# Optimization experiments

Measured on AMD Instinct MI355X. Metric: run time of the kernel, lower is better.

The kernel has to match this reference:

```python
import jax, jax.numpy as jnp
import numpy as np

N = 50000      # nodes
E = 1600000    # edges
F = 128        # num_feature
H = 256        # num_hidden
L = 3          # num_message_passing_steps
EPS = 1e-5     # LayerNorm eps (torch default)


def setup_inputs() -> dict:
    key = jax.random.key(0)
    ks = jax.random.split(key, 8)
    node = jax.random.normal(ks[0], (N, F), dtype=jnp.float32)
    edges = jax.random.randint(ks[1], (2, E), 0, N, dtype=jnp.int64)
    edges_attr = jax.random.uniform(ks[2], (E,), dtype=jnp.float32)
    sF = np.float32(1.0 / np.sqrt(F))
    sH = np.float32(1.0 / np.sqrt(H))
    W1 = jax.random.normal(ks[3], (F, H), dtype=jnp.float32) * sF
    b1 = jnp.zeros((H,), jnp.float32)
    W_convs = jax.random.normal(ks[4], (L, H, H), dtype=jnp.float32) * sH
    b_convs = jnp.zeros((L, H), jnp.float32)
    ln_g = jnp.ones((L, H), jnp.float32)
    ln_b = jnp.zeros((L, H), jnp.float32)
    fc_W = jax.random.normal(ks[5], (H, 2), dtype=jnp.float32) * sH
    fc_b = jnp.zeros((2,), jnp.float32)
    return dict(node=node, edges=edges, edges_attr=edges_attr, W1=W1, b1=b1,
                W_convs=W_convs, b_convs=b_convs, ln_g=ln_g, ln_b=ln_b,
                fc_W=fc_W, fc_b=fc_b)


def gcn_conv(x, src_a, dst_a, w_a, W, b):
    # PyG GCNConv: x' = D^-1/2 (A + I) D^-1/2 (x W) + b, edge weights w.
    # src_a/dst_a/w_a already include self-loops (weight 1).
    n = x.shape[0]
    xw = x @ W                                      # [N, H]
    deg = jax.ops.segment_sum(w_a, dst_a, num_segments=n)
    deg_safe = jnp.where(deg > 0, deg, 1.0)
    dinv = jnp.where(deg > 0, jax.lax.rsqrt(deg_safe), 0.0)
    norm = dinv[src_a] * w_a * dinv[dst_a]          # [E+N]
    msg = xw[src_a] * norm[:, None]                 # gather + scale
    out = jax.ops.segment_sum(msg, dst_a, num_segments=n)  # scatter-add
    return out + b


def layer_norm(x, g, b):
    mu = jnp.mean(x, axis=-1, keepdims=True)
    var = jnp.mean((x - mu) ** 2, axis=-1, keepdims=True)
    return (x - mu) * jax.lax.rsqrt(var + EPS) * g + b


def reference(node, edges, edges_attr, W1, b1, W_convs, b_convs, ln_g, ln_b, fc_W, fc_b):
    n = node.shape[0]
    loop = jnp.arange(n, dtype=edges.dtype)
    src_a = jnp.concatenate([edges[0], loop])
    dst_a = jnp.concatenate([edges[1], loop])
    w_a = jnp.concatenate([edges_attr, jnp.ones((n,), edges_attr.dtype)])

    x = gcn_conv(node, src_a, dst_a, w_a, W1, b1)
    for i in range(L):
        x_res = x
        x = gcn_conv(x, src_a, dst_a, w_a, W_convs[i], b_convs[i])
        x = layer_norm(x, ln_g[i], ln_b[i])
        x = jax.nn.relu(x + x_res)
    x = x @ fc_W + fc_b                              # [N, 2]
    return jnp.mean(x, axis=0, keepdims=True)        # global_mean_pool, batch=None -> [1, 2]
```

## Files before the change

### kernel.cpp

```cpp
#include <hip/hip_runtime.h>

#define EPS 1e-5f
#define FIXSCALE 8388608.0f

typedef __attribute__((ext_vector_type(8))) short short8;
typedef __attribute__((ext_vector_type(4))) short short4v;
typedef __attribute__((ext_vector_type(4))) float float4v;
typedef __attribute__((ext_vector_type(8))) unsigned short ushort8;
typedef __attribute__((ext_vector_type(4))) unsigned int uint4v;

#if __has_builtin(__builtin_nontemporal_load)
#define NT_LOAD(p) __builtin_nontemporal_load(p)
#else
#define NT_LOAD(p) (*(p))
#endif

__device__ __forceinline__ unsigned short f2b(float f) {
    union { float f; unsigned u; } v; v.f = f;
    unsigned r = v.u + 0x7FFF + ((v.u >> 16) & 1);
    return (unsigned short)(r >> 16);
}
__device__ __forceinline__ float b2f(unsigned short u) {
    union { unsigned u; float f; } v; v.u = ((unsigned)u) << 16;
    return v.f;
}


__global__ __launch_bounds__(256) void rank_kernel(const int* __restrict__ dst,
                                                   const float* __restrict__ w,
                                                   unsigned long long* __restrict__ combo,
                                                   int* __restrict__ rank, int E) {
    int e = blockIdx.x * 256 + threadIdx.x;
    if (e < E) {
        int d = dst[e];
        unsigned long long pack = (1ULL << 32) | (unsigned long long)(unsigned)(w[e] * FIXSCALE);
        unsigned long long old = atomicAdd(&combo[(size_t)d * 8], pack);
        rank[e] = (int)(old >> 32);
    }
}

__global__ __launch_bounds__(1024) void scan_dinv_kernel(const unsigned long long* __restrict__ combo,
                                                         int* __restrict__ row_ptr,
                                                         float* __restrict__ dinv, int n) {
    int tid = threadIdx.x, lane = tid & 63, w = tid >> 6;
    __shared__ int wsum[16];
    __shared__ int s_carry;
    if (tid == 0) s_carry = 0;
    __syncthreads();
    for (int base = 0; base < n; base += 1024) {
        int i = base + tid;
        int v = 0;
        if (i < n) {
            unsigned long long cb = combo[(size_t)i * 8];
            int cnt = (int)(cb >> 32);
            v = (cnt + 4) & ~3;
            float degv = (float)(unsigned)(cb & 0xffffffffULL) * (1.0f / FIXSCALE);
            dinv[i] = rsqrtf(degv + 1.0f);
        }
        int x = v;
        for (int off = 1; off < 64; off <<= 1) {
            int t = __shfl_up(x, off);
            if (lane >= off) x += t;
        }
        if (lane == 63) wsum[w] = x;
        __syncthreads();
        if (w == 0 && lane < 16) {
            int s = wsum[lane];
            for (int off = 1; off < 16; off <<= 1) {
                int t = __shfl_up(s, off, 16);
                if (lane >= off) s += t;
            }
            wsum[lane] = s;
        }
        __syncthreads();
        int carry = s_carry;
        int woff = (w > 0) ? wsum[w - 1] : 0;
        if (i < n) row_ptr[i + 1] = carry + woff + x;
        __syncthreads();
        if (tid == 0) s_carry = carry + wsum[15];
        __syncthreads();
    }
    if (tid == 0) row_ptr[0] = 0;
}

__global__ __launch_bounds__(256) void selfpad_kernel(const unsigned long long* __restrict__ combo,
                                                      const int* __restrict__ row_ptr,
                                                      const float* __restrict__ dinv,
                                                      unsigned int* __restrict__ edge, int n) {
    int d = blockIdx.x * 256 + threadIdx.x;
    if (d < n) {
        int cnt = (int)(combo[(size_t)d * 8] >> 32);
        int j0 = row_ptr[d], j1 = row_ptr[d + 1];
        float di = dinv[d];
        edge[j0] = ((unsigned)f2b(di * di) << 16) | (unsigned)d;
        for (int j = j0 + 1 + cnt; j < j1; ++j) edge[j] = (unsigned)d;
    }
}

__global__ __launch_bounds__(256) void scatter2_kernel(
    const int* __restrict__ src, const int* __restrict__ dst,
    const float* __restrict__ w, const int* __restrict__ rank,
    const int* __restrict__ row_ptr, const float* __restrict__ dinv,
    unsigned int* __restrict__ edge, int E) {
    int e = blockIdx.x * 256 + threadIdx.x;
    if (e < E) {
        int d = dst[e], s = src[e];
        float wn = dinv[s] * w[e] * dinv[d];
        edge[row_ptr[d] + 1 + rank[e]] = ((unsigned)f2b(wn) << 16) | (unsigned)s;
    }
}

__global__ __launch_bounds__(256) void cast_sliced_kernel(const float* __restrict__ in,
                                                          unsigned short* __restrict__ out,
                                                          int n, int F) {
    int idx = blockIdx.x * 256 + threadIdx.x;
    if (idx < n * (F / 4)) {
        int f4 = idx * 4;
        int r = f4 / F, f = f4 - r * F;
        float4 v = *(const float4*)&in[(size_t)r * F + f];
        short4v s = (short4v){(short)f2b(v.x), (short)f2b(v.y), (short)f2b(v.z), (short)f2b(v.w)};
        *(short4v*)&out[((size_t)(f >> 5) * n + r) * 32 + (f & 31)] = s;
    }
}

__global__ __launch_bounds__(256) void wtrans_kernel(const float* __restrict__ W,
                                                     unsigned short* __restrict__ Wt,
                                                     int K, int Nc) {
    int o = blockIdx.x * 256 + threadIdx.x;
    if (o < K * Nc) {
        int n = o / K, k = o - n * K;
        Wt[o] = f2b(W[(size_t)k * Nc + n]);
    }
}


#define GST 88

template <bool SLICEOUT>
__global__ __launch_bounds__(256) void gemm_n256(const unsigned short* __restrict__ A,
                                                 const unsigned short* __restrict__ Bt,
                                                 unsigned short* __restrict__ Cout,
                                                 const float* __restrict__ bias,
                                                 int M, int K) {
    __shared__ __align__(16) short As[64 * GST];
    __shared__ __align__(16) short Bs[256 * GST];
    int t = threadIdx.x;
    int lane = t & 63, w = t >> 6;
    int quad = lane >> 4, l16 = lane & 15;
    int row0 = blockIdx.x * 64;

    float4v acc[16];
#pragma unroll
    for (int c = 0; c < 16; ++c) acc[c] = (float4v){0.f, 0.f, 0.f, 0.f};

    int arow = t >> 2, ak16 = (t & 3) * 16;
    int bcol0 = t >> 2, bko = (t & 3) * 16;

    for (int k_outer = 0; k_outer < K; k_outer += 64) {
        bool rowok = (row0 + arow) < M;
        const unsigned short* ap = &A[(size_t)(row0 + arow) * K + k_outer + ak16];
        uint4 z = make_uint4(0, 0, 0, 0);
        uint4 u0 = rowok ? *(const uint4*)ap : z;
        uint4 u1 = rowok ? *(const uint4*)(ap + 8) : z;
        *(uint4*)&As[arow * GST + ak16] = u0;
        *(uint4*)&As[arow * GST + ak16 + 8] = u1;
#pragma unroll
        for (int cb = 0; cb < 4; ++cb) {
            int col = bcol0 + 64 * cb;
            const unsigned short* bp = &Bt[(size_t)col * K + k_outer + bko];
#pragma unroll
            for (int u = 0; u < 2; ++u)
                *(uint4*)&Bs[col * GST + bko + u * 8] = *(const uint4*)&bp[u * 8];
        }
        __syncthreads();
#pragma unroll
        for (int k0 = 0; k0 < 64; k0 += 32) {
            short8 a = *(const short8*)&As[(w * 16 + l16) * GST + k0 + quad * 8];
#pragma unroll
            for (int c = 0; c < 16; ++c) {
                short8 b = *(const short8*)&Bs[(c * 16 + l16) * GST + k0 + quad * 8];
                acc[c] = __builtin_amdgcn_mfma_f32_16x16x32_bf16(a, b, acc[c], 0, 0, 0);
            }
        }
        __syncthreads();
    }
#pragma unroll
    for (int c = 0; c < 16; ++c) {
        int col = c * 16 + l16;
        float bcol = (!SLICEOUT) ? bias[col] : 0.0f;
#pragma unroll
        for (int r = 0; r < 4; ++r) {
            int row = row0 + w * 16 + quad * 4 + r;
            if (row < M) {
                if (SLICEOUT)
                    Cout[((size_t)(c >> 1) * M + row) * 32 + ((c & 1) << 4) + l16] = f2b(acc[c][r]);
                else
                    Cout[(size_t)row * 256 + col] = f2b(acc[c][r] + bcol);
            }
        }
    }
}


#define CAPQ 1024

template <int CSH>
__global__ __launch_bounds__(256) void agg_grp(
    const unsigned short* __restrict__ tab0, const int* __restrict__ row_ptr,
    const unsigned int* __restrict__ edge, unsigned short* __restrict__ outb, int n) {
    __shared__ uint4v eq[CAPQ];
    int b = blockIdx.x;
    int s = b & ((1 << CSH) - 1);
    int grp = b >> CSH;
    int t = threadIdx.x;
    int d0 = grp * 64;
    int d = d0 + (t >> 2);

    const uint4v* e4p = (const uint4v*)edge;
    int qbase = row_ptr[d0] >> 2;
    int dmax = d0 + 64 < n ? d0 + 64 : n;
    int qcnt = (row_ptr[dmax] >> 2) - qbase;
    int qstage = qcnt < CAPQ ? qcnt : CAPQ;
    for (int i = t; i < qstage; i += 256) eq[i] = NT_LOAD(&e4p[qbase + i]);
    __syncthreads();

    if (d >= n) return;
    int fo = (t & 3) << 3;
    const unsigned short* tab = tab0 + (size_t)s * n * 32;

    int j = row_ptr[d] >> 2, j1 = row_ptr[d + 1] >> 2;
    int jmid = j1 < qbase + CAPQ ? j1 : qbase + CAPQ;

    float a[8] = {0.f, 0.f, 0.f, 0.f, 0.f, 0.f, 0.f, 0.f};

    auto process = [&](uint4v e4) {
#pragma unroll
        for (int u = 0; u < 4; ++u) {
            unsigned e = e4[u];
            float w = __int_as_float((int)(e & 0xffff0000u));
            unsigned off = ((e & 0xffffu) << 5) + (unsigned)fo;
            ushort8 r = *(const ushort8*)(tab + off);
#pragma unroll
            for (int k = 0; k < 8; ++k) a[k] += b2f(r[k]) * w;
        }
    };

    for (; j + 2 <= jmid; j += 2) {
        uint4v e4a = eq[j - qbase];
        uint4v e4b = eq[j + 1 - qbase];
        process(e4a);
        process(e4b);
    }
    if (j < jmid) { process(eq[j - qbase]); ++j; }
    for (; j < j1; ++j) process(NT_LOAD(&e4p[j]));

    ushort8 o;
#pragma unroll
    for (int k = 0; k < 8; ++k) o[k] = f2b(a[k]);
    *(ushort8*)(outb + ((size_t)d << (5 + CSH)) + (s << 5) + fo) = o;
}


__global__ __launch_bounds__(256) void ln_res_relu(
    const unsigned short* __restrict__ preln, const float* __restrict__ bias,
    const float* __restrict__ g, const float* __restrict__ lb,
    const unsigned short* __restrict__ res, unsigned short* __restrict__ out, int n) {
    int wv = __builtin_amdgcn_readfirstlane(threadIdx.x >> 6);
    int d = blockIdx.x * 4 + wv;
    if (d >= n) return;
    int l = threadIdx.x & 63;
    int fo = l * 4;
    ushort4 pv = *(const ushort4*)&preln[(size_t)d * 256 + fo];
    float4 bb = *(const float4*)&bias[fo];
    float v[4] = {b2f(pv.x) + bb.x, b2f(pv.y) + bb.y, b2f(pv.z) + bb.z, b2f(pv.w) + bb.w};
    float s4 = v[0] + v[1] + v[2] + v[3];
#pragma unroll
    for (int off = 1; off < 64; off <<= 1) s4 += __shfl_xor(s4, off);
    float mu = s4 * (1.0f / 256.0f);
    float dv[4];
    float qs = 0.f;
#pragma unroll
    for (int j = 0; j < 4; ++j) { dv[j] = v[j] - mu; qs += dv[j] * dv[j]; }
#pragma unroll
    for (int off = 1; off < 64; off <<= 1) qs += __shfl_xor(qs, off);
    float rs = rsqrtf(qs * (1.0f / 256.0f) + EPS);

    float4 gg = *(const float4*)&g[fo];
    float4 lbv = *(const float4*)&lb[fo];
    ushort4 rr4 = *(const ushort4*)&res[(size_t)d * 256 + fo];
    float ggv[4] = {gg.x, gg.y, gg.z, gg.w};
    float lbvv[4] = {lbv.x, lbv.y, lbv.z, lbv.w};
    float rrv[4] = {b2f(rr4.x), b2f(rr4.y), b2f(rr4.z), b2f(rr4.w)};
    ushort4 o;
    unsigned short* op = (unsigned short*)&o;
#pragma unroll
    for (int j = 0; j < 4; ++j) {
        float x = dv[j] * rs * ggv[j] + lbvv[j] + rrv[j];
        op[j] = f2b(x > 0.f ? x : 0.f);
    }
    *(ushort4*)&out[(size_t)d * 256 + fo] = o;
}


__global__ __launch_bounds__(256) void colsum_kernel(const unsigned short* __restrict__ x,
                                                     float* __restrict__ sums, int n) {
    int h = threadIdx.x;
    float acc = 0.0f;
    for (int r = blockIdx.x; r < n; r += gridDim.x) acc += b2f(x[(size_t)r * 256 + h]);
    atomicAdd(&sums[h], acc);
}

__global__ __launch_bounds__(64) void final_kernel(const float* __restrict__ sums,
                                                   const float* __restrict__ fcW,
                                                   const float* __restrict__ fcb,
                                                   float* __restrict__ out, float invN) {
    int lane = threadIdx.x;
    float p0 = 0.0f, p1 = 0.0f;
    for (int hh = lane; hh < 256; hh += 64) {
        float m = sums[hh];
        p0 += m * fcW[hh * 2 + 0];
        p1 += m * fcW[hh * 2 + 1];
    }
    for (int off = 32; off > 0; off >>= 1) {
        p0 += __shfl_down(p0, off);
        p1 += __shfl_down(p1, off);
    }
    if (lane == 0) {
        out[0] = p0 * invN + fcb[0];
        out[1] = p1 * invN + fcb[1];
    }
}


extern "C" void kernel_launch(void* const* d_in, const int* in_sizes, int n_in,
                              void* d_out, int out_size, void* d_ws, size_t ws_size,
                              hipStream_t stream) {
    const float* node    = (const float*)d_in[0];
    const int*   edges   = (const int*)d_in[1];
    const float* eattr   = (const float*)d_in[2];
    const float* W1      = (const float*)d_in[3];
    const float* b1      = (const float*)d_in[4];
    const float* W_convs = (const float*)d_in[5];
    const float* b_convs = (const float*)d_in[6];
    const float* ln_g    = (const float*)d_in[7];
    const float* ln_b    = (const float*)d_in[8];
    const float* fc_W    = (const float*)d_in[9];
    const float* fc_b    = (const float*)d_in[10];
    float* out = (float*)d_out;

    const int H = in_sizes[4];
    const int F = in_sizes[3] / H;
    const int N = in_sizes[0] / F;
    const int E = in_sizes[2];
    const int L = in_sizes[6] / H;

    const int* src = edges;
    const int* dst = edges + E;

    char* p = (char*)d_ws;
    auto alloc = [&](size_t bytes) {
        char* r = p;
        p += (bytes + 255) & ~(size_t)255;
        return r;
    };
    unsigned long long* combo = (unsigned long long*)alloc((size_t)N * 64);
    float* colsums = (float*)alloc((size_t)H * 4);
    size_t zero_bytes = (size_t)((char*)colsums - (char*)combo) + (((size_t)H * 4 + 255) & ~(size_t)255);
    float* dinv    = (float*)alloc((size_t)N * 4);
    int*   row_ptr = (int*)alloc((size_t)(N + 1) * 4);
    unsigned int* edge = (unsigned int*)alloc(((size_t)E + 4 * (size_t)N + 64) * 4);
    unsigned short* Wt1 = (unsigned short*)alloc((size_t)H * F * 2);
    unsigned short* Wtc = (unsigned short*)alloc((size_t)L * H * H * 2);
    unsigned short* xw  = (unsigned short*)alloc((size_t)N * H * 2);
    unsigned short* preln = (unsigned short*)alloc((size_t)N * H * 2);
    unsigned short* bufA  = (unsigned short*)alloc((size_t)N * H * 2);
    unsigned short* bufB  = (unsigned short*)alloc((size_t)N * H * 2);
    int*            rank  = (int*)xw;
    unsigned short* nodeb = preln;
    unsigned short* aggn  = preln + (size_t)N * F;

    hipMemsetAsync(combo, 0, zero_bytes, stream);

    int gE = (E + 255) / 256;
    int gN = (N + 255) / 256;
    rank_kernel<<<gE, 256, 0, stream>>>(dst, eattr, combo, rank, E);
    scan_dinv_kernel<<<1, 1024, 0, stream>>>(combo, row_ptr, dinv, N);
    selfpad_kernel<<<gN, 256, 0, stream>>>(combo, row_ptr, dinv, edge, N);
    scatter2_kernel<<<gE, 256, 0, stream>>>(src, dst, eattr, rank, row_ptr, dinv, edge, E);

    cast_sliced_kernel<<<(N * (F / 4) + 255) / 256, 256, 0, stream>>>(node, nodeb, N, F);
    wtrans_kernel<<<(F * H + 255) / 256, 256, 0, stream>>>(W1, Wt1, F, H);
    for (int i = 0; i < L; ++i)
        wtrans_kernel<<<(H * H + 255) / 256, 256, 0, stream>>>(
            W_convs + (size_t)i * H * H, Wtc + (size_t)i * H * H, H, H);

    int ngrp64 = (N + 63) / 64;
    int lngrid = (N + 3) / 4;
    int ggrid = (N + 63) / 64;

    agg_grp<2><<<4 * ngrp64, 256, 0, stream>>>(nodeb, row_ptr, edge, aggn, N);
    gemm_n256<false><<<ggrid, 256, 0, stream>>>(aggn, Wt1, bufA, b1, N, F);

    unsigned short* x = bufA;
    unsigned short* other = bufB;
    for (int i = 0; i < L; ++i) {
        gemm_n256<true><<<ggrid, 256, 0, stream>>>(x, Wtc + (size_t)i * H * H, xw, nullptr, N, H);
        agg_grp<3><<<8 * ngrp64, 256, 0, stream>>>(xw, row_ptr, edge, preln, N);
        ln_res_relu<<<lngrid, 256, 0, stream>>>(preln, b_convs + (size_t)i * H,
                                                ln_g + (size_t)i * H, ln_b + (size_t)i * H,
                                                x, other, N);
        unsigned short* t = x; x = other; other = t;
    }

    colsum_kernel<<<256, 256, 0, stream>>>(x, colsums, N);
    final_kernel<<<1, 64, 0, stream>>>(colsums, fc_W, fc_b, out, 1.0f / (float)N);
}
```

Before: 775.4 us.

## Sort destination nodes by degree bucket to balance aggregation warps; packed float2 accumulate

Adds a counting sort of destination nodes by padded in-degree, so the CSR rows are laid out in degree order and each aggregation wavefront handles nodes of similar length. This is meant to cut divergence and load imbalance in the gather loop. The aggregation writes each output row back to its original node index through the permutation. It also rewrites the bf16 unpack and multiply-accumulate as float2 vector operations, which the compiler may map to packed FMA. In exchange it adds three small preprocessing kernels (including a single-block scan), an extra indirection in the setup kernels, and scattered output writes from the aggregation.

After: 1.286 ms. 1.66x slower.

```diff
diff --git a/kernel.cpp b/kernel.cpp
--- a/kernel.cpp
+++ b/kernel.cpp
@@ -2,10 +2,12 @@
 
 #define EPS 1e-5f
 #define FIXSCALE 8388608.0f
+#define NB 512
 
 typedef __attribute__((ext_vector_type(8))) short short8;
 typedef __attribute__((ext_vector_type(4))) short short4v;
 typedef __attribute__((ext_vector_type(4))) float float4v;
+typedef __attribute__((ext_vector_type(2))) float float2v;
 typedef __attribute__((ext_vector_type(8))) unsigned short ushort8;
 typedef __attribute__((ext_vector_type(4))) unsigned int uint4v;
 
@@ -39,7 +41,51 @@
     }
 }
 
+
+__global__ __launch_bounds__(256) void bin_hist_kernel(const unsigned long long* __restrict__ combo,
+                                                       int* __restrict__ hist, int n) {
+    int d = blockIdx.x * 256 + threadIdx.x;
+    if (d < n) {
+        int cnt = (int)(combo[(size_t)d * 8] >> 32);
+        int qc = ((cnt + 4) & ~3) >> 2;
+        int b = qc < NB ? qc : NB - 1;
+        atomicAdd(&hist[b], 1);
+    }
+}
+
+__global__ __launch_bounds__(NB) void bucket_scan_kernel(const int* __restrict__ hist,
+                                                         int* __restrict__ cursor) {
+    __shared__ int v1[NB], v2[NB];
+    int t = threadIdx.x;
+    v1[t] = hist[t];
+    __syncthreads();
+    int* cur = v1; int* nxt = v2;
+    for (int off = 1; off < NB; off <<= 1) {
+        int x = cur[t] + ((t + off < NB) ? cur[t + off] : 0);
+        nxt[t] = x;
+        __syncthreads();
+        int* tmp = cur; cur = nxt; nxt = tmp;
+    }
+    cursor[t] = cur[t] - hist[t];
+}
+
+__global__ __launch_bounds__(256) void bin_scatter_kernel(const unsigned long long* __restrict__ combo,
+                                                          int* __restrict__ cursor,
+                                                          int* __restrict__ perm,
+                                                          int* __restrict__ posod, int n) {
+    int d = blockIdx.x * 256 + threadIdx.x;
+    if (d < n) {
+        int cnt = (int)(combo[(size_t)d * 8] >> 32);
+        int qc = ((cnt + 4) & ~3) >> 2;
+        int b = qc < NB ? qc : NB - 1;
+        int pos = atomicAdd(&cursor[b], 1);
+        perm[pos] = d;
+        posod[d] = pos;
+    }
+}
+
 __global__ __launch_bounds__(1024) void scan_dinv_kernel(const unsigned long long* __restrict__ combo,
+                                                         const int* __restrict__ perm,
                                                          int* __restrict__ row_ptr,
                                                          float* __restrict__ dinv, int n) {
     int tid = threadIdx.x, lane = tid & 63, w = tid >> 6;
@@ -52,10 +98,10 @@
         int v = 0;
         if (i < n) {
             unsigned long long cb = combo[(size_t)i * 8];
-            int cnt = (int)(cb >> 32);
-            v = (cnt + 4) & ~3;
             float degv = (float)(unsigned)(cb & 0xffffffffULL) * (1.0f / FIXSCALE);
             dinv[i] = rsqrtf(degv + 1.0f);
+            int cntp = (int)(combo[(size_t)perm[i] * 8] >> 32);
+            v = (cntp + 4) & ~3;
         }
         int x = v;
         for (int off = 1; off < 64; off <<= 1) {
@@ -85,12 +131,14 @@
 
 __global__ __launch_bounds__(256) void selfpad_kernel(const unsigned long long* __restrict__ combo,
                                                       const int* __restrict__ row_ptr,
+                                                      const int* __restrict__ posod,
                                                       const float* __restrict__ dinv,
                                                       unsigned int* __restrict__ edge, int n) {
     int d = blockIdx.x * 256 + threadIdx.x;
     if (d < n) {
         int cnt = (int)(combo[(size_t)d * 8] >> 32);
-        int j0 = row_ptr[d], j1 = row_ptr[d + 1];
+        int slot = posod[d];
+        int j0 = row_ptr[slot], j1 = row_ptr[slot + 1];
         float di = dinv[d];
         edge[j0] = ((unsigned)f2b(di * di) << 16) | (unsigned)d;
         for (int j = j0 + 1 + cnt; j < j1; ++j) edge[j] = (unsigned)d;
@@ -100,13 +148,13 @@
 __global__ __launch_bounds__(256) void scatter2_kernel(
     const int* __restrict__ src, const int* __restrict__ dst,
     const float* __restrict__ w, const int* __restrict__ rank,
-    const int* __restrict__ row_ptr, const float* __restrict__ dinv,
-    unsigned int* __restrict__ edge, int E) {
+    const int* __restrict__ row_ptr, const int* __restrict__ posod,
+    const float* __restrict__ dinv, unsigned int* __restrict__ edge, int E) {
     int e = blockIdx.x * 256 + threadIdx.x;
     if (e < E) {
         int d = dst[e], s = src[e];
         float wn = dinv[s] * w[e] * dinv[d];
-        edge[row_ptr[d] + 1 + rank[e]] = ((unsigned)f2b(wn) << 16) | (unsigned)s;
+        edge[row_ptr[posod[d]] + 1 + rank[e]] = ((unsigned)f2b(wn) << 16) | (unsigned)s;
     }
 }
 
@@ -207,7 +255,8 @@
 template <int CSH>
 __global__ __launch_bounds__(256) void agg_grp(
     const unsigned short* __restrict__ tab0, const int* __restrict__ row_ptr,
-    const unsigned int* __restrict__ edge, unsigned short* __restrict__ outb, int n) {
+    const int* __restrict__ perm, const unsigned int* __restrict__ edge,
+    unsigned short* __restrict__ outb, int n) {
     __shared__ uint4v eq[CAPQ];
     int b = blockIdx.x;
     int s = b & ((1 << CSH) - 1);
@@ -231,17 +280,27 @@
     int j = row_ptr[d] >> 2, j1 = row_ptr[d + 1] >> 2;
     int jmid = j1 < qbase + CAPQ ? j1 : qbase + CAPQ;
 
-    float a[8] = {0.f, 0.f, 0.f, 0.f, 0.f, 0.f, 0.f, 0.f};
+    float2v a2[4];
+#pragma unroll
+    for (int k = 0; k < 4; ++k) a2[k] = (float2v){0.f, 0.f};
 
     auto process = [&](uint4v e4) {
 #pragma unroll
         for (int u = 0; u < 4; ++u) {
             unsigned e = e4[u];
-            float w = __int_as_float((int)(e & 0xffff0000u));
+            float wq = __int_as_float((int)(e & 0xffff0000u));
+            float2v w2 = {wq, wq};
             unsigned off = ((e & 0xffffu) << 5) + (unsigned)fo;
-            ushort8 r = *(const ushort8*)(tab + off);
-#pragma unroll
-            for (int k = 0; k < 8; ++k) a[k] += b2f(r[k]) * w;
+            uint4 rr = *(const uint4*)(tab + off);
+            unsigned uu0 = rr.x, uu1 = rr.y, uu2 = rr.z, uu3 = rr.w;
+            float2v f0 = {__uint_as_float(uu0 << 16), __uint_as_float(uu0 & 0xffff0000u)};
+            float2v f1 = {__uint_as_float(uu1 << 16), __uint_as_float(uu1 & 0xffff0000u)};
+            float2v f2 = {__uint_as_float(uu2 << 16), __uint_as_float(uu2 & 0xffff0000u)};
+            float2v f3 = {__uint_as_float(uu3 << 16), __uint_as_float(uu3 & 0xffff0000u)};
+            a2[0] += f0 * w2;
+            a2[1] += f1 * w2;
+            a2[2] += f2 * w2;
+            a2[3] += f3 * w2;
         }
     };
 
@@ -254,10 +313,14 @@
     if (j < jmid) { process(eq[j - qbase]); ++j; }
     for (; j < j1; ++j) process(NT_LOAD(&e4p[j]));
 
+    int p = perm[d];
     ushort8 o;
 #pragma unroll
-    for (int k = 0; k < 8; ++k) o[k] = f2b(a[k]);
-    *(ushort8*)(outb + ((size_t)d << (5 + CSH)) + (s << 5) + fo) = o;
+    for (int k = 0; k < 4; ++k) {
+        o[2 * k] = f2b(a2[k].x);
+        o[2 * k + 1] = f2b(a2[k].y);
+    }
+    *(ushort8*)(outb + ((size_t)p << (5 + CSH)) + (s << 5) + fo) = o;
 }
 
 
@@ -365,7 +428,11 @@
     };
     unsigned long long* combo = (unsigned long long*)alloc((size_t)N * 64);
     float* colsums = (float*)alloc((size_t)H * 4);
-    size_t zero_bytes = (size_t)((char*)colsums - (char*)combo) + (((size_t)H * 4 + 255) & ~(size_t)255);
+    int*   hist    = (int*)alloc((size_t)NB * 4);
+    size_t zero_bytes = (size_t)((char*)hist - (char*)combo) + (((size_t)NB * 4 + 255) & ~(size_t)255);
+    int*   cursor  = (int*)alloc((size_t)NB * 4);
+    int*   perm    = (int*)alloc((size_t)N * 4);
+    int*   posod   = (int*)alloc((size_t)N * 4);
     float* dinv    = (float*)alloc((size_t)N * 4);
     int*   row_ptr = (int*)alloc((size_t)(N + 1) * 4);
     unsigned int* edge = (unsigned int*)alloc(((size_t)E + 4 * (size_t)N + 64) * 4);
@@ -384,9 +451,12 @@
     int gE = (E + 255) / 256;
     int gN = (N + 255) / 256;
     rank_kernel<<<gE, 256, 0, stream>>>(dst, eattr, combo, rank, E);
-    scan_dinv_kernel<<<1, 1024, 0, stream>>>(combo, row_ptr, dinv, N);
-    selfpad_kernel<<<gN, 256, 0, stream>>>(combo, row_ptr, dinv, edge, N);
-    scatter2_kernel<<<gE, 256, 0, stream>>>(src, dst, eattr, rank, row_ptr, dinv, edge, E);
+    bin_hist_kernel<<<gN, 256, 0, stream>>>(combo, hist, N);
+    bucket_scan_kernel<<<1, NB, 0, stream>>>(hist, cursor);
+    bin_scatter_kernel<<<gN, 256, 0, stream>>>(combo, cursor, perm, posod, N);
+    scan_dinv_kernel<<<1, 1024, 0, stream>>>(combo, perm, row_ptr, dinv, N);
+    selfpad_kernel<<<gN, 256, 0, stream>>>(combo, row_ptr, posod, dinv, edge, N);
+    scatter2_kernel<<<gE, 256, 0, stream>>>(src, dst, eattr, rank, row_ptr, posod, dinv, edge, E);
 
     cast_sliced_kernel<<<(N * (F / 4) + 255) / 256, 256, 0, stream>>>(node, nodeb, N, F);
     wtrans_kernel<<<(F * H + 255) / 256, 256, 0, stream>>>(W1, Wt1, F, H);
@@ -398,14 +468,14 @@
     int lngrid = (N + 3) / 4;
     int ggrid = (N + 63) / 64;
 
-    agg_grp<2><<<4 * ngrp64, 256, 0, stream>>>(nodeb, row_ptr, edge, aggn, N);
+    agg_grp<2><<<4 * ngrp64, 256, 0, stream>>>(nodeb, row_ptr, perm, edge, aggn, N);
     gemm_n256<false><<<ggrid, 256, 0, stream>>>(aggn, Wt1, bufA, b1, N, F);
 
     unsigned short* x = bufA;
     unsigned short* other = bufB;
     for (int i = 0; i < L; ++i) {
         gemm_n256<true><<<ggrid, 256, 0, stream>>>(x, Wtc + (size_t)i * H * H, xw, nullptr, N, H);
-        agg_grp<3><<<8 * ngrp64, 256, 0, stream>>>(xw, row_ptr, edge, preln, N);
+        agg_grp<3><<<8 * ngrp64, 256, 0, stream>>>(xw, row_ptr, perm, edge, preln, N);
         ln_res_relu<<<lngrid, 256, 0, stream>>>(preln, b_convs + (size_t)i * H,
                                                 ln_g + (size_t)i * H, ln_b + (size_t)i * H,
                                                 x, other, N);
```
